# Kernel optimization log

Hardware: AMD Instinct MI355X
Metric: run time of the kernel (lower is better)

The kernel has to match this reference:

```python
import jax, jax.numpy as jnp
from jax import lax
import numpy as np

BOHR = 0.52917721067  # Angstrom per Bohr (au.BOHR)
DAMP_MUTUAL = 0.39
DAMP_FIELD = 0.7
N_ITER = 7  # fixed-point iterations for induced dipoles


def setup_inputs() -> dict:
    key = jax.random.key(0)
    N = 100000
    deg = 32
    E = N * deg
    k1, k2, k3, k4, k5, k6, k7 = jax.random.split(key, 7)
    edge_src = jax.random.randint(k1, (E,), 0, N)
    edge_dst = jax.random.randint(k2, (E,), 0, N)
    # realistic interatomic distances in [1, 6] Angstrom (avoid r ~ 0)
    distances = 1.0 + 5.0 * jax.random.uniform(k3, (E,), dtype=jnp.float32)
    u = jax.random.normal(k4, (E, 3), dtype=jnp.float32)
    u = u / jnp.linalg.norm(u, axis=-1, keepdims=True)
    vec = u * distances[:, None]  # consistent |vec| == distances
    polarisability = 0.5 + 1.5 * jax.random.uniform(k5, (N,), dtype=jnp.float32)
    charges = 0.3 * jax.random.normal(k6, (N,), dtype=jnp.float32)
    species = jax.random.randint(k7, (N,), 1, 10)
    return {
        "species": species,
        "edge_src": edge_src,
        "edge_dst": edge_dst,
        "distances": distances,
        "vec": vec,
        "polarisability": polarisability,
        "charges": charges,
    }


def reference(species, edge_src, edge_dst, distances, vec, polarisability, charges):
    N = polarisability.shape[0]
    # convert to atomic units
    rij = distances / BOHR                      # [E]
    vec_ij = vec / BOHR                         # [E,3]
    pol = polarisability.reshape(-1) / BOHR**3  # [N]

    # Thole damping: u_ij^3 = r^3 / sqrt(alpha_i * alpha_j)
    alpha_ij = pol[edge_src] * pol[edge_dst]
    uij3 = rij**3 / jnp.sqrt(alpha_ij)
    exp_m = jnp.exp(-DAMP_MUTUAL * uij3)
    l3_m = 1.0 - exp_m
    l5_m = 1.0 - (1.0 + DAMP_MUTUAL * uij3) * exp_m
    l3_f = 1.0 - jnp.exp(-DAMP_FIELD * uij3)

    inv_r3 = 1.0 / rij**3
    inv_r5 = inv_r3 / rij**2

    # permanent (charge) electric field at src atoms, Thole-damped
    e_edges = (l3_f * charges[edge_dst] * inv_r3)[:, None] * vec_ij  # [E,3]
    E0 = jax.ops.segment_sum(e_edges, edge_src, num_segments=N)      # [N,3]

    alpha = pol[:, None]  # isotropic polarisability [N,1]

    def matvec(mu):
        # Thole-damped dipole-dipole interaction tensor applied to mu: (T mu)_i
        mu_d = mu[edge_dst]                                   # [E,3]
        dot = jnp.sum(vec_ij * mu_d, axis=-1)                 # [E]
        t = (l3_m * inv_r3)[:, None] * mu_d \
            - (3.0 * l5_m * inv_r5 * dot)[:, None] * vec_ij   # [E,3]
        return jax.ops.segment_sum(t, edge_src, num_segments=N)

    # iterative induced dipoles: mu = alpha * (E0 - T mu)
    mu0 = alpha * E0

    def step(mu, _):
        return alpha * (E0 - matvec(mu)), None

    mu, _ = lax.scan(step, mu0, None, length=N_ITER)

    # per-atom polarisation energy: -1/2 mu . E0
    energy = -0.5 * jnp.sum(mu * E0, axis=-1)  # [N]
    return energy
```

## Files before the change

kernel.cpp:

```cpp
#include <hip/hip_runtime.h>
#include <hip/hip_fp16.h>


static constexpr float INV_B  = 1.0f / 0.52917721067f;
static constexpr float INV_B3 = INV_B * INV_B * INV_B;
static constexpr float DM = 0.39f;
static constexpr float DF = 0.7f;
static constexpr int   NITER = 7;
#define SCAN_B 1024
#define STAGE 2048
#define BUILD_T 1024
#define MAXBUCK 512

__device__ inline unsigned packh2(float a, float b) {
    return (unsigned)__half_as_ushort(__float2half_rn(a)) |
           ((unsigned)__half_as_ushort(__float2half_rn(b)) << 16);
}
__device__ inline float unph_lo(unsigned u) {
    return __half2float(__ushort_as_half((unsigned short)(u & 0xFFFFu)));
}
__device__ inline float unph_hi(unsigned u) {
    return __half2float(__ushort_as_half((unsigned short)(u >> 16)));
}


__global__ void bhist_kernel(const int* __restrict__ esrc, int* __restrict__ hraw,
                             int* __restrict__ hpad, int E, int nbuck, int nblk, int chunk)
{
    __shared__ int cnt[MAXBUCK];
    int tid = threadIdx.x, blk = blockIdx.x;
    for (int b = tid; b < nbuck; b += blockDim.x) cnt[b] = 0;
    __syncthreads();
    int lo = blk * chunk, hi = min(E, lo + chunk);
    for (int i = lo + tid; i < hi; i += blockDim.x)
        atomicAdd(&cnt[esrc[i] >> 8], 1);
    __syncthreads();
    for (int b = tid; b < nbuck; b += blockDim.x) {
        int c = cnt[b];
        hraw[b * nblk + blk] = c;
        hpad[b * nblk + blk] = (c + 7) & ~7;
    }
}


__global__ void scan1_kernel(const int* __restrict__ in, int* __restrict__ excl,
                             int* __restrict__ blocksum, int n)
{
    __shared__ int sh[SCAN_B];
    int tid = threadIdx.x;
    int i = blockIdx.x * SCAN_B + tid;
    int v = (i < n) ? in[i] : 0;
    sh[tid] = v;
    __syncthreads();
    for (int off = 1; off < SCAN_B; off <<= 1) {
        int t = (tid >= off) ? sh[tid - off] : 0;
        __syncthreads();
        sh[tid] += t;
        __syncthreads();
    }
    if (i < n) excl[i] = sh[tid] - v;
    if (tid == SCAN_B - 1) blocksum[blockIdx.x] = sh[tid];
}

__global__ void scan2_kernel(int* __restrict__ blocksum, int nb)
{
    __shared__ int sh[1024];
    int tid = threadIdx.x;
    int v = (tid < nb) ? blocksum[tid] : 0;
    sh[tid] = v;
    __syncthreads();
    for (int off = 1; off < 1024; off <<= 1) {
        int t = (tid >= off) ? sh[tid - off] : 0;
        __syncthreads();
        sh[tid] += t;
        __syncthreads();
    }
    if (tid < nb) blocksum[tid] = sh[tid] - v;
}

__global__ void scan3_kernel(int* __restrict__ excl, const int* __restrict__ blocksum, int n)
{
    int i = blockIdx.x * SCAN_B + threadIdx.x;
    if (i < n) excl[i] += blocksum[blockIdx.x];
}

__global__ void bktptr_kernel(const int* __restrict__ hoffpad, const int* __restrict__ hpad,
                              int* __restrict__ bktptr, int nbuck, int nblk, int nScan)
{
    int b = blockIdx.x * blockDim.x + threadIdx.x;
    if (b < nbuck) bktptr[b] = hoffpad[b * nblk];
    if (b == nbuck) bktptr[b] = hoffpad[nScan - 1] + hpad[nScan - 1];
}


__global__ __launch_bounds__(BUILD_T)
void build_kernel(const int* __restrict__ esrc, const int* __restrict__ edst,
                  const float* __restrict__ dist, const float* __restrict__ vec,
                  const float* __restrict__ pol, const float* __restrict__ chg,
                  const int* __restrict__ hoffpad, const int* __restrict__ hpad,
                  uint4* __restrict__ recs, int E, int nbuck, int nblk, int chunk)
{
    __shared__ uint4 stg[STAGE];
    __shared__ unsigned short sbuck[STAGE];
    __shared__ int wcur[MAXBUCK];
    __shared__ int shist[MAXBUCK];
    __shared__ int sscan[MAXBUCK];
    __shared__ int scur[MAXBUCK];
    int tid = threadIdx.x, blk = blockIdx.x;
    int lo = blk * chunk, hi = min(E, lo + chunk), cnt = hi - lo;

    for (int b = tid; b < nbuck; b += BUILD_T) wcur[b] = hoffpad[b * nblk + blk];
    __syncthreads();

    int nsb = (cnt + STAGE - 1) / STAGE;
    for (int sb = 0; sb < nsb; ++sb) {
        int s0 = sb * STAGE, s1 = min(cnt, s0 + STAGE), scnt = s1 - s0;
        for (int b = tid; b < nbuck; b += BUILD_T) shist[b] = 0;
        __syncthreads();
        for (int i = s0 + tid; i < s1; i += BUILD_T)
            atomicAdd(&shist[esrc[lo + i] >> 8], 1);
        __syncthreads();
        if (tid < MAXBUCK) sscan[tid] = (tid < nbuck) ? shist[tid] : 0;
        __syncthreads();
        for (int off = 1; off < MAXBUCK; off <<= 1) {
            int t = 0;
            if (tid < MAXBUCK && tid >= off) t = sscan[tid - off];
            __syncthreads();
            if (tid < MAXBUCK) sscan[tid] += t;
            __syncthreads();
        }
        if (tid < nbuck) {
            int ex = sscan[tid] - shist[tid];
            sscan[tid] = ex;
            scur[tid]  = ex;
        }
        __syncthreads();
        for (int i = s0 + tid; i < s1; i += BUILD_T) {
            int gi = lo + i;
            int s = esrc[gi], d = edst[gi];
            int b = s >> 8;
            float r  = dist[gi] * INV_B;
            float vx = vec[3*gi+0] * INV_B;
            float vy = vec[3*gi+1] * INV_B;
            float vz = vec[3*gi+2] * INV_B;
            float ps = pol[s] * INV_B3;
            float pd = pol[d] * INV_B3;
            float r2 = r * r;
            float r3 = r2 * r;
            float u  = r3 * rsqrtf(ps * pd);
            float em = __expf(-DM * u);
            float l3m = 1.0f - em;
            float l5m = 1.0f - (1.0f + DM * u) * em;
            float inv_r3 = 1.0f / r3;
            float inv_r5 = inv_r3 / r2;
            float c1 = l3m * inv_r3;
            float sw = sqrtf(3.0f * l5m * inv_r5);
            float ec = (1.0f - __expf(-DF * u)) * chg[d] * inv_r3;
            float g  = ec / sw;
            uint4 rc;
            rc.x = (unsigned)(d | ((s & 255) << 20));
            rc.y = __float_as_uint(c1);
            rc.z = packh2(sw * vx, sw * vy);
            rc.w = packh2(sw * vz, g);
            int sl = atomicAdd(&scur[b], 1);
            stg[sl]   = rc;
            sbuck[sl] = (unsigned short)b;
        }
        __syncthreads();
        for (int k = tid; k < scnt; k += BUILD_T) {
            int b = sbuck[k];
            recs[wcur[b] + (k - sscan[b])] = stg[k];
        }
        __syncthreads();
        for (int b = tid; b < nbuck; b += BUILD_T) wcur[b] += shist[b];
        __syncthreads();
    }
    for (int b = tid; b < nbuck; b += BUILD_T) {
        int base = hoffpad[b * nblk + blk];
        int end  = base + hpad[b * nblk + blk];
        for (int s2 = wcur[b]; s2 < end; ++s2) recs[s2] = make_uint4(0, 0, 0, 0);
    }
}


__global__ void sort_kernel(const int* __restrict__ bktptr, const int* __restrict__ hoffraw,
                            int nblk, const uint4* __restrict__ recs_raw,
                            unsigned* __restrict__ srt, float* __restrict__ gsrt,
                            int* __restrict__ rowbeg, int* __restrict__ rowend, int N)
{
    __shared__ int hist[256];
    __shared__ int scn[256];
    __shared__ int cur[256];
    int tid = threadIdx.x, b = blockIdx.x;
    int j0 = bktptr[b], j1 = bktptr[b + 1];
    int tight0 = hoffraw[b * nblk];
    if (tid < 256) hist[tid] = 0;
    __syncthreads();
    for (int j = j0 + tid; j < j1; j += blockDim.x) {
        uint4 rc = recs_raw[j];
        if (rc.y) atomicAdd(&hist[rc.x >> 20], 1);
    }
    __syncthreads();
    if (tid < 256) scn[tid] = hist[tid];
    __syncthreads();
    for (int off = 1; off < 256; off <<= 1) {
        int t = 0;
        if (tid < 256 && tid >= off) t = scn[tid - off];
        __syncthreads();
        if (tid < 256) scn[tid] += t;
        __syncthreads();
    }
    if (tid < 256) {
        int c = hist[tid];
        int beg = tight0 + scn[tid] - c;
        cur[tid] = beg;
        int row = b * 256 + tid;
        if (row < N) { rowbeg[row] = beg; rowend[row] = beg + c; }
    }
    __syncthreads();
    for (int j = j0 + tid; j < j1; j += blockDim.x) {
        uint4 rc = recs_raw[j];
        if (rc.y) {
            int slot = atomicAdd(&cur[rc.x >> 20], 1);
            float c1 = __uint_as_float(rc.y);
            srt[3*slot+0] = rc.x;
            srt[3*slot+1] = packh2(c1, unph_lo(rc.z));
            srt[3*slot+2] = packh2(unph_hi(rc.z), unph_lo(rc.w));
            gsrt[slot] = unph_hi(rc.w);
        }
    }
}


__global__ void e0g_kernel(const int* __restrict__ rowbeg, const int* __restrict__ rowend,
                           const unsigned* __restrict__ srt, const float* __restrict__ gsrt,
                           const float* __restrict__ pol,
                           float4* __restrict__ E0, float4* __restrict__ mu, int N)
{
    int tid  = threadIdx.x;
    int lane = tid & 15;
    int row  = (blockIdx.x * blockDim.x + tid) >> 4;
    if (row >= N) return;
    int r0 = rowbeg[row], r1 = rowend[row];
    float sx = 0.f, sy = 0.f, sz = 0.f;
    for (int j = r0 + lane; j < r1; j += 16) {
        unsigned w0 = srt[3*j+1];
        unsigned w1 = srt[3*j+2];
        float g = gsrt[j];
        sx += g * unph_hi(w0);
        sy += g * unph_lo(w1);
        sz += g * unph_hi(w1);
    }
    for (int m = 8; m >= 1; m >>= 1) {
        sx += __shfl_xor(sx, m);
        sy += __shfl_xor(sy, m);
        sz += __shfl_xor(sz, m);
    }
    if (lane == 0) {
        E0[row] = make_float4(sx, sy, sz, 0.f);
        float a = pol[row] * INV_B3;
        mu[row] = make_float4(a * sx, a * sy, a * sz, 0.f);
    }
}

__global__ void mvg_kernel(const int* __restrict__ rowbeg, const int* __restrict__ rowend,
                           const unsigned* __restrict__ srt, const float4* __restrict__ E0,
                           const float* __restrict__ pol,
                           const float4* __restrict__ mu_in, float4* __restrict__ mu_out,
                           float* __restrict__ energy, int N, int final_iter)
{
    int tid  = threadIdx.x;
    int lane = tid & 15;
    int row  = (blockIdx.x * blockDim.x + tid) >> 4;
    if (row >= N) return;
    int r0 = rowbeg[row], r1 = rowend[row];
    float ax = 0.f, ay = 0.f, az = 0.f;
    for (int j = r0 + lane; j < r1; j += 16) {
        unsigned pk = srt[3*j+0];
        unsigned w0 = srt[3*j+1];
        unsigned w1 = srt[3*j+2];
        float4 m = mu_in[pk & 0xFFFFF];
        float c1 = unph_lo(w0);
        float wx = unph_hi(w0), wy = unph_lo(w1), wz = unph_hi(w1);
        float dot = wx * m.x + wy * m.y + wz * m.z;
        ax += c1 * m.x - dot * wx;
        ay += c1 * m.y - dot * wy;
        az += c1 * m.z - dot * wz;
    }
    for (int msk = 8; msk >= 1; msk >>= 1) {
        ax += __shfl_xor(ax, msk);
        ay += __shfl_xor(ay, msk);
        az += __shfl_xor(az, msk);
    }
    if (lane == 0) {
        float4 e0 = E0[row];
        float a = pol[row] * INV_B3;
        float mx = a * (e0.x - ax);
        float my = a * (e0.y - ay);
        float mz = a * (e0.z - az);
        mu_out[row] = make_float4(mx, my, mz, 0.f);
        if (final_iter)
            energy[row] = -0.5f * (mx * e0.x + my * e0.y + mz * e0.z);
    }
}


__global__ void e0b_kernel(const int* __restrict__ bktptr, const uint4* __restrict__ recs,
                           const float* __restrict__ pol,
                           float4* __restrict__ E0, float4* __restrict__ mu, int N)
{
    __shared__ float acc[256 * 3];
    int tid = threadIdx.x, b = blockIdx.x;
    for (int k = tid; k < 768; k += 256) acc[k] = 0.f;
    __syncthreads();
    int j0 = bktptr[b], j1 = bktptr[b + 1];
    for (int j = j0 + tid; j < j1; j += 256) {
        uint4 rc = recs[j];
        int lr = (int)(rc.x >> 20) & 255;
        float g = unph_hi(rc.w);
        atomicAdd(&acc[lr*3+0], g * unph_lo(rc.z));
        atomicAdd(&acc[lr*3+1], g * unph_hi(rc.z));
        atomicAdd(&acc[lr*3+2], g * unph_lo(rc.w));
    }
    __syncthreads();
    int r = b * 256 + tid;
    if (r < N) {
        float ax = acc[tid*3], ay = acc[tid*3+1], az = acc[tid*3+2];
        E0[r] = make_float4(ax, ay, az, 0.f);
        float a = pol[r] * INV_B3;
        mu[r] = make_float4(a * ax, a * ay, a * az, 0.f);
    }
}

__global__ void mvb_kernel(const int* __restrict__ bktptr, const uint4* __restrict__ recs,
                           const float4* __restrict__ E0, const float* __restrict__ pol,
                           const float4* __restrict__ mu_in, float4* __restrict__ mu_out,
                           float* __restrict__ energy, int N, int final_iter)
{
    __shared__ float acc[256 * 3];
    int tid = threadIdx.x, b = blockIdx.x;
    for (int k = tid; k < 768; k += 256) acc[k] = 0.f;
    __syncthreads();
    int j0 = bktptr[b], j1 = bktptr[b + 1];
    for (int j = j0 + tid; j < j1; j += 256) {
        uint4 rc = recs[j];
        float4 m = mu_in[rc.x & 0xFFFFF];
        float c1 = __uint_as_float(rc.y);
        float wx = unph_lo(rc.z), wy = unph_hi(rc.z), wz = unph_lo(rc.w);
        float dot = wx * m.x + wy * m.y + wz * m.z;
        int lr = (int)(rc.x >> 20) & 255;
        atomicAdd(&acc[lr*3+0], c1 * m.x - dot * wx);
        atomicAdd(&acc[lr*3+1], c1 * m.y - dot * wy);
        atomicAdd(&acc[lr*3+2], c1 * m.z - dot * wz);
    }
    __syncthreads();
    int r = b * 256 + tid;
    if (r < N) {
        float4 e0 = E0[r];
        float a = pol[r] * INV_B3;
        float mx = a * (e0.x - acc[tid*3+0]);
        float my = a * (e0.y - acc[tid*3+1]);
        float mz = a * (e0.z - acc[tid*3+2]);
        mu_out[r] = make_float4(mx, my, mz, 0.f);
        if (final_iter)
            energy[r] = -0.5f * (mx * e0.x + my * e0.y + mz * e0.z);
    }
}


__global__ void fb_e0_kernel(const int* esrc, const int* edst, const float* dist,
                             const float* vec, const float* pol, const float* chg,
                             float4* E0, int E)
{
    int e = blockIdx.x * blockDim.x + threadIdx.x;
    if (e >= E) return;
    int s = esrc[e], d = edst[e];
    float r  = dist[e] * INV_B;
    float vx = vec[3*e+0]*INV_B, vy = vec[3*e+1]*INV_B, vz = vec[3*e+2]*INV_B;
    float r3 = r*r*r;
    float u  = r3 * rsqrtf(pol[s]*INV_B3 * pol[d]*INV_B3);
    float ec = (1.0f - __expf(-DF*u)) * chg[d] / r3;
    atomicAdd(&E0[s].x, ec*vx); atomicAdd(&E0[s].y, ec*vy); atomicAdd(&E0[s].z, ec*vz);
}

__global__ void fb_init_kernel(const float* pol, const float4* E0, float4* mu, float4* acc, int N)
{
    int i = blockIdx.x * blockDim.x + threadIdx.x;
    if (i >= N) return;
    float a = pol[i]*INV_B3; float4 e0 = E0[i];
    mu[i]  = make_float4(a*e0.x, a*e0.y, a*e0.z, 0.f);
    acc[i] = make_float4(0.f,0.f,0.f,0.f);
}

__global__ void fb_matvec_kernel(const int* esrc, const int* edst, const float* dist,
                                 const float* vec, const float* pol,
                                 const float4* mu, float4* acc, int E)
{
    int e = blockIdx.x * blockDim.x + threadIdx.x;
    if (e >= E) return;
    int s = esrc[e], d = edst[e];
    float r  = dist[e]*INV_B;
    float vx = vec[3*e+0]*INV_B, vy = vec[3*e+1]*INV_B, vz = vec[3*e+2]*INV_B;
    float r2 = r*r, r3 = r2*r;
    float u  = r3 * rsqrtf(pol[s]*INV_B3 * pol[d]*INV_B3);
    float em = __expf(-DM*u);
    float c1 = (1.0f - em) / r3;
    float c2 = 3.0f * (1.0f - (1.0f + DM*u)*em) / (r3*r2);
    float4 m = mu[d];
    float k = c2 * (vx*m.x + vy*m.y + vz*m.z);
    atomicAdd(&acc[s].x, c1*m.x - k*vx);
    atomicAdd(&acc[s].y, c1*m.y - k*vy);
    atomicAdd(&acc[s].z, c1*m.z - k*vz);
}

__global__ void fb_update_kernel(const float* pol, const float4* E0, float4* acc,
                                 float4* mu, float* energy, int N, int final_iter)
{
    int i = blockIdx.x * blockDim.x + threadIdx.x;
    if (i >= N) return;
    float a = pol[i]*INV_B3; float4 e0 = E0[i]; float4 ac = acc[i];
    float mx = a*(e0.x-ac.x), my = a*(e0.y-ac.y), mz = a*(e0.z-ac.z);
    mu[i]  = make_float4(mx,my,mz,0.f);
    acc[i] = make_float4(0.f,0.f,0.f,0.f);
    if (final_iter) energy[i] = -0.5f*(mx*e0.x + my*e0.y + mz*e0.z);
}


static inline size_t align_up(size_t x, size_t a) { return (x + a - 1) & ~(a - 1); }

struct Layout {
    int chunk, nblk, nScan, g1;
    size_t o_hpad, o_hoffpad, o_bsum1, o_bkt, o_E0, o_mua, o_mub, o_hraw, o_recsraw;
    size_t need_mid;
    size_t o_hoffraw, o_bsum2, o_rowbeg, o_rowend, o_srt, o_gsrt;
    size_t need_sort;
};

static Layout make_layout(int E, int N, int nbuck, int chunk)
{
    Layout L;
    L.chunk = chunk;
    L.nblk  = (E + chunk - 1) / chunk;
    L.nScan = nbuck * L.nblk;
    L.g1    = (L.nScan + SCAN_B - 1) / SCAN_B;
    size_t Epad = (size_t)E + 7u * (size_t)L.nScan;
    size_t off = 0;
    auto carve = [&](size_t bytes) { size_t o = off; off = align_up(off + bytes, 256); return o; };
    L.o_hpad    = carve((size_t)L.nScan * 4);
    L.o_hoffpad = carve((size_t)L.nScan * 4);
    L.o_bsum1   = carve(1024 * 4);
    L.o_bkt     = carve((size_t)(nbuck + 1) * 4);
    L.o_E0      = carve((size_t)N * 16);
    L.o_mua     = carve((size_t)N * 16);
    L.o_mub     = carve((size_t)N * 16);
    L.o_hraw    = carve((size_t)L.nScan * 4);
    L.o_recsraw = carve(Epad * 16);
    L.need_mid  = off;
    L.o_hoffraw = carve((size_t)L.nScan * 4);
    L.o_bsum2   = carve(1024 * 4);
    L.o_rowbeg  = carve((size_t)N * 4);
    L.o_rowend  = carve((size_t)N * 4);
    L.o_srt     = carve((size_t)E * 12);
    L.o_gsrt    = carve((size_t)E * 4);
    L.need_sort = off;
    return L;
}

extern "C" void kernel_launch(void* const* d_in, const int* in_sizes, int n_in,
                              void* d_out, int out_size, void* d_ws, size_t ws_size,
                              hipStream_t stream)
{
    const int*   esrc = (const int*)  d_in[1];
    const int*   edst = (const int*)  d_in[2];
    const float* dist = (const float*)d_in[3];
    const float* vec  = (const float*)d_in[4];
    const float* pol  = (const float*)d_in[5];
    const float* chg  = (const float*)d_in[6];
    const int E = in_sizes[1];
    const int N = in_sizes[5];
    float* out = (float*)d_out;

    const int nbuck = (N + 255) >> 8;

    const int cand[3] = {8192, 16384, 32768};
    Layout L{}; bool ok_sort = false, ok_mid = false;
    for (int ci = 0; ci < 3; ++ci) {
        Layout t = make_layout(E, N, nbuck, cand[ci]);
        bool shp = (nbuck <= MAXBUCK) && (t.g1 <= 1024) && (nbuck >= 1) && (N < (1 << 20));
        if (shp && ws_size >= t.need_sort) { L = t; ok_sort = true; break; }
    }
    if (!ok_sort) {
        Layout t = make_layout(E, N, nbuck, 32768);
        bool shp = (nbuck <= MAXBUCK) && (t.g1 <= 1024) && (nbuck >= 1) && (N < (1 << 20));
        if (shp && ws_size >= t.need_mid) { L = t; ok_mid = true; }
    }

    char* ws = (char*)d_ws;

    if (ok_sort || ok_mid) {
        int*    hpad    = (int*)   (ws + L.o_hpad);
        int*    hoffpad = (int*)   (ws + L.o_hoffpad);
        int*    bsum1   = (int*)   (ws + L.o_bsum1);
        int*    bktptr  = (int*)   (ws + L.o_bkt);
        float4* E0      = (float4*)(ws + L.o_E0);
        float4* mu_a    = (float4*)(ws + L.o_mua);
        float4* mu_b    = (float4*)(ws + L.o_mub);
        int*    hraw    = (int*)   (ws + L.o_hraw);
        uint4*  recsraw = (uint4*) (ws + L.o_recsraw);

        bhist_kernel<<<L.nblk, BUILD_T, 0, stream>>>(esrc, hraw, hpad, E, nbuck,
                                                     L.nblk, L.chunk);
        scan1_kernel<<<L.g1, SCAN_B, 0, stream>>>(hpad, hoffpad, bsum1, L.nScan);
        scan2_kernel<<<1, 1024, 0, stream>>>(bsum1, L.g1);
        scan3_kernel<<<L.g1, SCAN_B, 0, stream>>>(hoffpad, bsum1, L.nScan);
        bktptr_kernel<<<(nbuck + 256) / 256, 256, 0, stream>>>(hoffpad, hpad, bktptr,
                                                               nbuck, L.nblk, L.nScan);
        build_kernel<<<L.nblk, BUILD_T, 0, stream>>>(esrc, edst, dist, vec, pol, chg,
                                                     hoffpad, hpad, recsraw,
                                                     E, nbuck, L.nblk, L.chunk);

        if (ok_sort) {
            int*      hoffraw = (int*)     (ws + L.o_hoffraw);
            int*      bsum2   = (int*)     (ws + L.o_bsum2);
            int*      rowbeg  = (int*)     (ws + L.o_rowbeg);
            int*      rowend  = (int*)     (ws + L.o_rowend);
            unsigned* srt     = (unsigned*)(ws + L.o_srt);
            float*    gsrt    = (float*)   (ws + L.o_gsrt);

            scan1_kernel<<<L.g1, SCAN_B, 0, stream>>>(hraw, hoffraw, bsum2, L.nScan);
            scan2_kernel<<<1, 1024, 0, stream>>>(bsum2, L.g1);
            scan3_kernel<<<L.g1, SCAN_B, 0, stream>>>(hoffraw, bsum2, L.nScan);
            sort_kernel<<<nbuck, 512, 0, stream>>>(bktptr, hoffraw, L.nblk, recsraw,
                                                   srt, gsrt, rowbeg, rowend, N);

            const int NG16 = (N + 15) / 16;
            e0g_kernel<<<NG16, 256, 0, stream>>>(rowbeg, rowend, srt, gsrt, pol, E0, mu_a, N);
            float4* min_ = mu_a; float4* mout_ = mu_b;
            for (int it = 0; it < NITER; ++it) {
                mvg_kernel<<<NG16, 256, 0, stream>>>(rowbeg, rowend, srt, E0, pol,
                                                     min_, mout_, out, N, it == NITER - 1);
                float4* t = min_; min_ = mout_; mout_ = t;
            }
        } else {
            e0b_kernel<<<nbuck, 256, 0, stream>>>(bktptr, recsraw, pol, E0, mu_a, N);
            float4* min_ = mu_a; float4* mout_ = mu_b;
            for (int it = 0; it < NITER; ++it) {
                mvb_kernel<<<nbuck, 256, 0, stream>>>(bktptr, recsraw, E0, pol,
                                                      min_, mout_, out, N, it == NITER - 1);
                float4* t = min_; min_ = mout_; mout_ = t;
            }
        }
    } else {
        float4* E0  = (float4*)(ws);
        float4* mu  = (float4*)(ws + (size_t)N * 16);
        float4* acc = (float4*)(ws + (size_t)N * 32);
        const int EB = 256, NB = 256;
        const int EG = (E + EB - 1) / EB;
        const int NG = (N + NB - 1) / NB;
        hipMemsetAsync(E0, 0, (size_t)N * 16, stream);
        fb_e0_kernel<<<EG, EB, 0, stream>>>(esrc, edst, dist, vec, pol, chg, E0, E);
        fb_init_kernel<<<NG, NB, 0, stream>>>(pol, E0, mu, acc, N);
        for (int it = 0; it < NITER; ++it) {
            fb_matvec_kernel<<<EG, EB, 0, stream>>>(esrc, edst, dist, vec, pol, mu, acc, E);
            fb_update_kernel<<<NG, NB, 0, stream>>>(pol, E0, acc, mu, out, N, it == NITER - 1);
        }
    }
}
```

Baseline: 335.0 us.

## Fuse E0 accumulation into sort kernel, use CSR rowptr, wave-shuffle bucket scan

The separate E0 pass is folded into the sort kernel. Each edge's field contribution is accumulated per row with shared-memory float atomics, and E0 and the initial mu are written at the end, which removes a kernel launch and the gsrt array round-trip. The rowbeg/rowend arrays become a single CSR rowptr, so mvg reads less index data. The build kernel drops to 512 threads and replaces its barrier-heavy Hillis-Steele bucket scan with a wave shuffle scan plus a small cross-wave scan. Risks: shared atomics on hot rows can contend, and float atomic ordering changes rounding slightly.

```diff
diff --git a/kernel.cpp b/kernel.cpp
--- a/kernel.cpp
+++ b/kernel.cpp
@@ -9,7 +9,7 @@
 static constexpr int   NITER = 7;
 #define SCAN_B 1024
 #define STAGE 2048
-#define BUILD_T 1024
+#define BUILD_T 512
 #define MAXBUCK 512
 
 __device__ inline unsigned packh2(float a, float b) {
@@ -85,11 +85,15 @@
 }
 
 __global__ void bktptr_kernel(const int* __restrict__ hoffpad, const int* __restrict__ hpad,
-                              int* __restrict__ bktptr, int nbuck, int nblk, int nScan)
+                              int* __restrict__ bktptr, int* __restrict__ rowptr,
+                              int nbuck, int nblk, int nScan, int N, int E)
 {
     int b = blockIdx.x * blockDim.x + threadIdx.x;
     if (b < nbuck) bktptr[b] = hoffpad[b * nblk];
-    if (b == nbuck) bktptr[b] = hoffpad[nScan - 1] + hpad[nScan - 1];
+    if (b == nbuck) {
+        bktptr[b] = hoffpad[nScan - 1] + hpad[nScan - 1];
+        if (rowptr) rowptr[N] = E;
+    }
 }
 
 
@@ -104,34 +108,47 @@
     __shared__ unsigned short sbuck[STAGE];
     __shared__ int wcur[MAXBUCK];
     __shared__ int shist[MAXBUCK];
-    __shared__ int sscan[MAXBUCK];
+    __shared__ int sbase[MAXBUCK];
     __shared__ int scur[MAXBUCK];
+    __shared__ int wsum[8];
     int tid = threadIdx.x, blk = blockIdx.x;
+    int lane = tid & 63, wav = tid >> 6;
     int lo = blk * chunk, hi = min(E, lo + chunk), cnt = hi - lo;
 
-    for (int b = tid; b < nbuck; b += BUILD_T) wcur[b] = hoffpad[b * nblk + blk];
+    if (tid < nbuck) wcur[tid] = hoffpad[tid * nblk + blk];
     __syncthreads();
 
     int nsb = (cnt + STAGE - 1) / STAGE;
     for (int sb = 0; sb < nsb; ++sb) {
         int s0 = sb * STAGE, s1 = min(cnt, s0 + STAGE), scnt = s1 - s0;
-        for (int b = tid; b < nbuck; b += BUILD_T) shist[b] = 0;
+        if (tid < nbuck) shist[tid] = 0;
         __syncthreads();
         for (int i = s0 + tid; i < s1; i += BUILD_T)
             atomicAdd(&shist[esrc[lo + i] >> 8], 1);
         __syncthreads();
-        if (tid < MAXBUCK) sscan[tid] = (tid < nbuck) ? shist[tid] : 0;
-        __syncthreads();
-        for (int off = 1; off < MAXBUCK; off <<= 1) {
-            int t = 0;
-            if (tid < MAXBUCK && tid >= off) t = sscan[tid - off];
-            __syncthreads();
-            if (tid < MAXBUCK) sscan[tid] += t;
-            __syncthreads();
-        }
+        int v = (tid < nbuck) ? shist[tid] : 0;
+        int x = v;
+        #pragma unroll
+        for (int off = 1; off < 64; off <<= 1) {
+            int t = __shfl_up(x, off);
+            if (lane >= off) x += t;
+        }
+        if (lane == 63) wsum[wav] = x;
+        __syncthreads();
+        if (tid < 8) {
+            int w = wsum[tid];
+            #pragma unroll
+            for (int off = 1; off < 8; off <<= 1) {
+                int t = __shfl_up(w, off, 8);
+                if (tid >= off) w += t;
+            }
+            wsum[tid] = w;
+        }
+        __syncthreads();
+        int base = (wav > 0) ? wsum[wav - 1] : 0;
         if (tid < nbuck) {
-            int ex = sscan[tid] - shist[tid];
-            sscan[tid] = ex;
+            int ex = x + base - v;
+            sbase[tid] = ex;
             scur[tid]  = ex;
         }
         __syncthreads();
@@ -169,32 +186,35 @@
         __syncthreads();
         for (int k = tid; k < scnt; k += BUILD_T) {
             int b = sbuck[k];
-            recs[wcur[b] + (k - sscan[b])] = stg[k];
-        }
-        __syncthreads();
-        for (int b = tid; b < nbuck; b += BUILD_T) wcur[b] += shist[b];
-        __syncthreads();
-    }
-    for (int b = tid; b < nbuck; b += BUILD_T) {
-        int base = hoffpad[b * nblk + blk];
-        int end  = base + hpad[b * nblk + blk];
-        for (int s2 = wcur[b]; s2 < end; ++s2) recs[s2] = make_uint4(0, 0, 0, 0);
+            recs[wcur[b] + (k - sbase[b])] = stg[k];
+        }
+        __syncthreads();
+        if (tid < nbuck) wcur[tid] += shist[tid];
+        __syncthreads();
+    }
+    if (tid < nbuck) {
+        int base = hoffpad[tid * nblk + blk];
+        int end  = base + hpad[tid * nblk + blk];
+        for (int s2 = wcur[tid]; s2 < end; ++s2) recs[s2] = make_uint4(0, 0, 0, 0);
     }
 }
 
 
 __global__ void sort_kernel(const int* __restrict__ bktptr, const int* __restrict__ hoffraw,
                             int nblk, const uint4* __restrict__ recs_raw,
-                            unsigned* __restrict__ srt, float* __restrict__ gsrt,
-                            int* __restrict__ rowbeg, int* __restrict__ rowend, int N)
+                            unsigned* __restrict__ srt,
+                            int* __restrict__ rowptr, const float* __restrict__ pol,
+                            float4* __restrict__ E0, float4* __restrict__ mu, int N)
 {
     __shared__ int hist[256];
     __shared__ int scn[256];
     __shared__ int cur[256];
+    __shared__ float acc[256 * 3];
     int tid = threadIdx.x, b = blockIdx.x;
     int j0 = bktptr[b], j1 = bktptr[b + 1];
     int tight0 = hoffraw[b * nblk];
     if (tid < 256) hist[tid] = 0;
+    for (int k = tid; k < 768; k += blockDim.x) acc[k] = 0.f;
     __syncthreads();
     for (int j = j0 + tid; j < j1; j += blockDim.x) {
         uint4 rc = recs_raw[j];
@@ -215,65 +235,49 @@
         int beg = tight0 + scn[tid] - c;
         cur[tid] = beg;
         int row = b * 256 + tid;
-        if (row < N) { rowbeg[row] = beg; rowend[row] = beg + c; }
+        if (row < N) rowptr[row] = beg;
     }
     __syncthreads();
     for (int j = j0 + tid; j < j1; j += blockDim.x) {
         uint4 rc = recs_raw[j];
         if (rc.y) {
-            int slot = atomicAdd(&cur[rc.x >> 20], 1);
+            int lr = (int)(rc.x >> 20);
+            int slot = atomicAdd(&cur[lr], 1);
             float c1 = __uint_as_float(rc.y);
+            float wx = unph_lo(rc.z), wy = unph_hi(rc.z);
+            float wz = unph_lo(rc.w), g  = unph_hi(rc.w);
             srt[3*slot+0] = rc.x;
-            srt[3*slot+1] = packh2(c1, unph_lo(rc.z));
-            srt[3*slot+2] = packh2(unph_hi(rc.z), unph_lo(rc.w));
-            gsrt[slot] = unph_hi(rc.w);
-        }
-    }
-}
-
-
-__global__ void e0g_kernel(const int* __restrict__ rowbeg, const int* __restrict__ rowend,
-                           const unsigned* __restrict__ srt, const float* __restrict__ gsrt,
+            srt[3*slot+1] = packh2(c1, wx);
+            srt[3*slot+2] = packh2(wy, wz);
+            atomicAdd(&acc[lr*3+0], g * wx);
+            atomicAdd(&acc[lr*3+1], g * wy);
+            atomicAdd(&acc[lr*3+2], g * wz);
+        }
+    }
+    __syncthreads();
+    if (tid < 256) {
+        int row = b * 256 + tid;
+        if (row < N) {
+            float ax = acc[tid*3], ay = acc[tid*3+1], az = acc[tid*3+2];
+            E0[row] = make_float4(ax, ay, az, 0.f);
+            float a = pol[row] * INV_B3;
+            mu[row] = make_float4(a * ax, a * ay, a * az, 0.f);
+        }
+    }
+}
+
+
+__global__ void mvg_kernel(const int* __restrict__ rowptr,
+                           const unsigned* __restrict__ srt, const float4* __restrict__ E0,
                            const float* __restrict__ pol,
-                           float4* __restrict__ E0, float4* __restrict__ mu, int N)
+                           const float4* __restrict__ mu_in, float4* __restrict__ mu_out,
+                           float* __restrict__ energy, int N, int final_iter)
 {
     int tid  = threadIdx.x;
     int lane = tid & 15;
     int row  = (blockIdx.x * blockDim.x + tid) >> 4;
     if (row >= N) return;
-    int r0 = rowbeg[row], r1 = rowend[row];
-    float sx = 0.f, sy = 0.f, sz = 0.f;
-    for (int j = r0 + lane; j < r1; j += 16) {
-        unsigned w0 = srt[3*j+1];
-        unsigned w1 = srt[3*j+2];
-        float g = gsrt[j];
-        sx += g * unph_hi(w0);
-        sy += g * unph_lo(w1);
-        sz += g * unph_hi(w1);
-    }
-    for (int m = 8; m >= 1; m >>= 1) {
-        sx += __shfl_xor(sx, m);
-        sy += __shfl_xor(sy, m);
-        sz += __shfl_xor(sz, m);
-    }
-    if (lane == 0) {
-        E0[row] = make_float4(sx, sy, sz, 0.f);
-        float a = pol[row] * INV_B3;
-        mu[row] = make_float4(a * sx, a * sy, a * sz, 0.f);
-    }
-}
-
-__global__ void mvg_kernel(const int* __restrict__ rowbeg, const int* __restrict__ rowend,
-                           const unsigned* __restrict__ srt, const float4* __restrict__ E0,
-                           const float* __restrict__ pol,
-                           const float4* __restrict__ mu_in, float4* __restrict__ mu_out,
-                           float* __restrict__ energy, int N, int final_iter)
-{
-    int tid  = threadIdx.x;
-    int lane = tid & 15;
-    int row  = (blockIdx.x * blockDim.x + tid) >> 4;
-    if (row >= N) return;
-    int r0 = rowbeg[row], r1 = rowend[row];
+    int r0 = rowptr[row], r1 = rowptr[row + 1];
     float ax = 0.f, ay = 0.f, az = 0.f;
     for (int j = r0 + lane; j < r1; j += 16) {
         unsigned pk = srt[3*j+0];
@@ -432,7 +436,7 @@
     int chunk, nblk, nScan, g1;
     size_t o_hpad, o_hoffpad, o_bsum1, o_bkt, o_E0, o_mua, o_mub, o_hraw, o_recsraw;
     size_t need_mid;
-    size_t o_hoffraw, o_bsum2, o_rowbeg, o_rowend, o_srt, o_gsrt;
+    size_t o_hoffraw, o_bsum2, o_rowptr, o_srt;
     size_t need_sort;
 };
 
@@ -458,10 +462,8 @@
     L.need_mid  = off;
     L.o_hoffraw = carve((size_t)L.nScan * 4);
     L.o_bsum2   = carve(1024 * 4);
-    L.o_rowbeg  = carve((size_t)N * 4);
-    L.o_rowend  = carve((size_t)N * 4);
+    L.o_rowptr  = carve((size_t)(N + 1) * 4);
     L.o_srt     = carve((size_t)E * 12);
-    L.o_gsrt    = carve((size_t)E * 4);
     L.need_sort = off;
     return L;
 }
@@ -507,6 +509,7 @@
         float4* mu_b    = (float4*)(ws + L.o_mub);
         int*    hraw    = (int*)   (ws + L.o_hraw);
         uint4*  recsraw = (uint4*) (ws + L.o_recsraw);
+        int*    rowptr  = ok_sort ? (int*)(ws + L.o_rowptr) : nullptr;
 
         bhist_kernel<<<L.nblk, BUILD_T, 0, stream>>>(esrc, hraw, hpad, E, nbuck,
                                                      L.nblk, L.chunk);
@@ -514,7 +517,8 @@
         scan2_kernel<<<1, 1024, 0, stream>>>(bsum1, L.g1);
         scan3_kernel<<<L.g1, SCAN_B, 0, stream>>>(hoffpad, bsum1, L.nScan);
         bktptr_kernel<<<(nbuck + 256) / 256, 256, 0, stream>>>(hoffpad, hpad, bktptr,
-                                                               nbuck, L.nblk, L.nScan);
+                                                               rowptr, nbuck, L.nblk,
+                                                               L.nScan, N, E);
         build_kernel<<<L.nblk, BUILD_T, 0, stream>>>(esrc, edst, dist, vec, pol, chg,
                                                      hoffpad, hpad, recsraw,
                                                      E, nbuck, L.nblk, L.chunk);
@@ -522,22 +526,18 @@
         if (ok_sort) {
             int*      hoffraw = (int*)     (ws + L.o_hoffraw);
             int*      bsum2   = (int*)     (ws + L.o_bsum2);
-            int*      rowbeg  = (int*)     (ws + L.o_rowbeg);
-            int*      rowend  = (int*)     (ws + L.o_rowend);
             unsigned* srt     = (unsigned*)(ws + L.o_srt);
-            float*    gsrt    = (float*)   (ws + L.o_gsrt);
 
             scan1_kernel<<<L.g1, SCAN_B, 0, stream>>>(hraw, hoffraw, bsum2, L.nScan);
             scan2_kernel<<<1, 1024, 0, stream>>>(bsum2, L.g1);
             scan3_kernel<<<L.g1, SCAN_B, 0, stream>>>(hoffraw, bsum2, L.nScan);
             sort_kernel<<<nbuck, 512, 0, stream>>>(bktptr, hoffraw, L.nblk, recsraw,
-                                                   srt, gsrt, rowbeg, rowend, N);
+                                                   srt, rowptr, pol, E0, mu_a, N);
 
             const int NG16 = (N + 15) / 16;
-            e0g_kernel<<<NG16, 256, 0, stream>>>(rowbeg, rowend, srt, gsrt, pol, E0, mu_a, N);
             float4* min_ = mu_a; float4* mout_ = mu_b;
             for (int it = 0; it < NITER; ++it) {
-                mvg_kernel<<<NG16, 256, 0, stream>>>(rowbeg, rowend, srt, E0, pol,
+                mvg_kernel<<<NG16, 256, 0, stream>>>(rowptr, srt, E0, pol,
                                                      min_, mout_, out, N, it == NITER - 1);
                 float4* t = min_; min_ = mout_; mout_ = t;
             }
```

Result: no change. 333.1 us (-0.6%).
